# Optimization experiments

Hardware: AMD Instinct MI355X
Metric: run time of the kernel (lower is better)

The kernel has to match this reference:

```python
import jax, jax.numpy as jnp
import numpy as np

N, H, F, E, K = 2048, 1024, 4096, 8, 2


def setup_inputs() -> dict:
    key = jax.random.key(0)
    ks = jax.random.split(key, 6)
    x = jax.random.normal(ks[0], (N, H), dtype=jnp.float32)
    mapping = jax.random.randint(ks[1], (N, K), 0, E)
    Wg = jax.random.normal(ks[2], (E, H), dtype=jnp.float32) * (1.0 / np.sqrt(H))
    W1 = jax.random.normal(ks[3], (E, H, F), dtype=jnp.float32) * (1.0 / np.sqrt(H))
    b1 = jnp.zeros((E, F), dtype=jnp.float32)
    W2 = jax.random.normal(ks[4], (E, F, H), dtype=jnp.float32) * (1.0 / np.sqrt(F))
    b2 = jnp.zeros((E, H), dtype=jnp.float32)
    return {"x": x, "mapping": mapping, "Wg": Wg, "W1": W1, "b1": b1, "W2": W2, "b2": b2}


def reference(x, mapping, Wg, W1, b1, W2, b2):
    # Gate logits: note original applies softmax over dim=0 (the token axis).
    logits = jax.nn.softmax(x @ Wg.T, axis=0)  # [N, E]

    # Per-expert MLP. Original sorts tokens by expert, runs per-expert GEMMs on
    # dynamic splits, then unsorts -- mathematically: y[i,k] = MLP_{mapping[i,k]}(x[i]).
    # JIT-friendly dense baseline: run every expert over all tokens, gather per token.
    def mlp(e):
        h = jax.nn.gelu(x @ W1[e] + b1[e])  # [N, F]
        return h @ W2[e] + b2[e]            # [N, H]

    y_all = jnp.stack([mlp(e) for e in range(E)])  # [E, N, H]

    # Gate weights gathered per (token, k), normalized over top-k.
    w = jnp.take_along_axis(logits, mapping, axis=1)  # [N, K]
    w = w / jnp.sum(w, axis=-1, keepdims=True)

    idx = jnp.arange(x.shape[0])
    out = jnp.zeros_like(x)
    for k in range(mapping.shape[1]):
        yk = y_all[mapping[:, k], idx]  # [N, H] gather per token's k-th expert
        out = out + yk * w[:, k:k + 1]
    return out
```

## Files before the change

kernel.cpp:

```cpp
#include <hip/hip_runtime.h>

#define N_TOK 2048
#define HD    1024
#define FD    4096
#define NE    8

typedef __attribute__((ext_vector_type(8))) short short8;
typedef __attribute__((ext_vector_type(4))) float floatx4;

__device__ __forceinline__ unsigned short f2bf(float f) {
  unsigned int u = __float_as_uint(f);
  u += 0x7fffu + ((u >> 16) & 1u);
  return (unsigned short)(u >> 16);
}

__device__ __forceinline__ void gl2lds16(const unsigned short* g, unsigned short* l) {
  __builtin_amdgcn_global_load_lds(
      (const __attribute__((address_space(1))) unsigned int*)g,
      (__attribute__((address_space(3))) unsigned int*)l, 16, 0, 0);
}

__device__ __forceinline__ float gelu_tanh(float x) {
  float t = 0.7978845608028654f * x * (1.0f + 0.044715f * x * x);
  return 0.5f * x * (1.0f + tanhf(t));
}

__device__ __forceinline__ int poff_of(const int* __restrict__ cnt, int e) {
  int o = 0;
  for (int i = 0; i < e; ++i) o += (cnt[i] + 127) & ~127;
  return o;
}

__global__ void k_gating(const float* __restrict__ x, const float* __restrict__ wg,
                         float* __restrict__ p) {
  int wave = threadIdx.x >> 6;
  int lane = threadIdx.x & 63;
  int n = blockIdx.x * 4 + wave;
  const float4* xr = (const float4*)(x + (size_t)n * HD);
  float4 xv[4];
  #pragma unroll
  for (int i = 0; i < 4; ++i) xv[i] = xr[lane + i * 64];
  for (int e = 0; e < NE; ++e) {
    const float4* wr = (const float4*)(wg + (size_t)e * HD);
    float s = 0.f;
    #pragma unroll
    for (int i = 0; i < 4; ++i) {
      float4 w4 = wr[lane + i * 64];
      s += xv[i].x * w4.x + xv[i].y * w4.y + xv[i].z * w4.z + xv[i].w * w4.w;
    }
    for (int o = 32; o > 0; o >>= 1) s += __shfl_xor(s, o, 64);
    if (lane == 0) p[e * N_TOK + n] = s;
  }
}

__global__ void k_softmax(float* __restrict__ p) {
  int e = blockIdx.x;
  float* col = p + e * N_TOK;
  __shared__ float red[256];
  int t = threadIdx.x;
  float m = -1e30f;
  for (int i = t; i < N_TOK; i += 256) m = fmaxf(m, col[i]);
  red[t] = m; __syncthreads();
  for (int s = 128; s > 0; s >>= 1) { if (t < s) red[t] = fmaxf(red[t], red[t + s]); __syncthreads(); }
  m = red[0]; __syncthreads();
  float sum = 0.f;
  for (int i = t; i < N_TOK; i += 256) { float v = expf(col[i] - m); col[i] = v; sum += v; }
  red[t] = sum; __syncthreads();
  for (int s = 128; s > 0; s >>= 1) { if (t < s) red[t] += red[t + s]; __syncthreads(); }
  float inv = 1.0f / red[0];
  for (int i = t; i < N_TOK; i += 256) col[i] *= inv;
}

__global__ void k_route(const int* __restrict__ mp, const float* __restrict__ p,
                        int* __restrict__ cnt, int* __restrict__ idxl,
                        int* __restrict__ tke, int* __restrict__ tks, float* __restrict__ tkw) {
  int n = blockIdx.x * 256 + threadIdx.x;
  if (n >= N_TOK) return;
  int m0 = mp[n * 2 + 0], m1 = mp[n * 2 + 1];
  if (m0 == m1) {
    int s = atomicAdd(&cnt[m0], 1);
    idxl[m0 * N_TOK + s] = n;
    tke[n * 2] = m0; tks[n * 2] = s; tkw[n * 2] = 1.0f;
    tke[n * 2 + 1] = m0; tks[n * 2 + 1] = s; tkw[n * 2 + 1] = 0.0f;
  } else {
    float p0 = p[m0 * N_TOK + n], p1 = p[m1 * N_TOK + n];
    float inv = 1.0f / (p0 + p1);
    int s0 = atomicAdd(&cnt[m0], 1);
    idxl[m0 * N_TOK + s0] = n;
    tke[n * 2] = m0; tks[n * 2] = s0; tkw[n * 2] = p0 * inv;
    int s1 = atomicAdd(&cnt[m1], 1);
    idxl[m1 * N_TOK + s1] = n;
    tke[n * 2 + 1] = m1; tks[n * 2 + 1] = s1; tkw[n * 2 + 1] = p1 * inv;
  }
}

__global__ void k_gather(const float* __restrict__ x, const int* __restrict__ cnt,
                         const int* __restrict__ idxl, unsigned short* __restrict__ xg) {
  int e = blockIdx.y;
  int r = blockIdx.x;
  int c = cnt[e];
  int pc = (c + 127) & ~127;
  if (r >= pc) return;
  unsigned short* dst = xg + ((size_t)poff_of(cnt, e) + r) * HD;
  int t = threadIdx.x;
  union { unsigned short us[8]; uint4 v; } o;
  if (r < c) {
    const float* src = x + (size_t)idxl[e * N_TOK + r] * HD;
    float4 f0 = ((const float4*)src)[t * 2];
    float4 f1 = ((const float4*)src)[t * 2 + 1];
    o.us[0] = f2bf(f0.x); o.us[1] = f2bf(f0.y); o.us[2] = f2bf(f0.z); o.us[3] = f2bf(f0.w);
    o.us[4] = f2bf(f1.x); o.us[5] = f2bf(f1.y); o.us[6] = f2bf(f1.z); o.us[7] = f2bf(f1.w);
  } else {
    o.v.x = 0u; o.v.y = 0u; o.v.z = 0u; o.v.w = 0u;
  }
  ((uint4*)dst)[t] = o.v;
}

__global__ __launch_bounds__(256) void k_transcvt2(const float* __restrict__ w1,
                                                   unsigned short* __restrict__ w1t,
                                                   const float* __restrict__ w2,
                                                   unsigned short* __restrict__ w2t) {
  __shared__ float tile[64][65];
  int l = blockIdx.x;
  const float* src; unsigned short* dst; int rows, cols, bx, by, e;
  if (l < 8192) {
    src = w1; dst = w1t; rows = HD; cols = FD;
    bx = l & 63; by = (l >> 6) & 15; e = l >> 10;
  } else {
    int l2 = l - 8192;
    src = w2; dst = w2t; rows = FD; cols = HD;
    bx = l2 & 15; by = (l2 >> 4) & 63; e = l2 >> 10;
  }
  const size_t base = (size_t)e * rows * cols;
  int c0 = bx * 64, r0 = by * 64;
  int t = threadIdx.x;
  int lr = t >> 4;
  int lc = (t & 15) * 4;
  #pragma unroll
  for (int i = 0; i < 64; i += 16) {
    float4 v = *(const float4*)(src + base + (size_t)(r0 + lr + i) * cols + c0 + lc);
    tile[lr + i][lc] = v.x; tile[lr + i][lc + 1] = v.y;
    tile[lr + i][lc + 2] = v.z; tile[lr + i][lc + 3] = v.w;
  }
  __syncthreads();
  int oc = t >> 2;
  int rseg = (t & 3) * 16;
  union { unsigned short us[16]; uint4 v[2]; } o;
  #pragma unroll
  for (int i = 0; i < 16; ++i) o.us[i] = f2bf(tile[rseg + i][oc]);
  unsigned short* d = dst + base + (size_t)(c0 + oc) * rows + r0 + rseg;
  ((uint4*)d)[0] = o.v[0];
  ((uint4*)d)[1] = o.v[1];
}

__global__ __launch_bounds__(256) void k_gemm1(
    const unsigned short* __restrict__ xg, const unsigned short* __restrict__ w1t,
    const float* __restrict__ b1, const int* __restrict__ cnt,
    unsigned short* __restrict__ h) {
  const int l = blockIdx.x;
  const int mt = l >> 5;
  const int nt = l & 31;
  const int mbase = mt * 128;
  const int nbase = nt * 128;

  int e = -1;
  {
    int o = 0;
    #pragma unroll
    for (int i = 0; i < NE; ++i) {
      int ci = cnt[i];
      int pc = (ci + 127) & ~127;
      if (mbase >= o && mbase < o + pc) e = i;
      o += pc;
    }
  }
  if (e < 0) return;

  const unsigned short* A = xg + (size_t)mbase * HD;
  const unsigned short* B = w1t + ((size_t)e * FD + nbase) * HD;

  __shared__ unsigned short As[128 * 32];
  __shared__ unsigned short Bs[128 * 32];

  const int tid = threadIdx.x;
  const int wave = tid >> 6, lane = tid & 63;
  const int quad = lane >> 4, lrow = lane & 15;
  const int wm = (wave >> 1) * 64, wn = (wave & 1) * 64;

  floatx4 acc[4][4];
  #pragma unroll
  for (int i = 0; i < 4; ++i)
    #pragma unroll
    for (int j = 0; j < 4; ++j) acc[i][j] = (floatx4){0.f, 0.f, 0.f, 0.f};

  const int r0 = tid >> 2, k0 = (tid & 3) * 8;

  for (int kt = 0; kt < HD / 32; ++kt) {
    __syncthreads();
    const unsigned short* ga = A + kt * 32;
    const unsigned short* gb = B + kt * 32;
    gl2lds16(ga + (size_t)r0 * HD + k0,        As + (size_t)(wave * 64) * 8);
    gl2lds16(ga + (size_t)(64 + r0) * HD + k0, As + (size_t)(256 + wave * 64) * 8);
    gl2lds16(gb + (size_t)r0 * HD + k0,        Bs + (size_t)(wave * 64) * 8);
    gl2lds16(gb + (size_t)(64 + r0) * HD + k0, Bs + (size_t)(256 + wave * 64) * 8);
    __syncthreads();
    short8 aF[4], bF[4];
    #pragma unroll
    for (int i = 0; i < 4; ++i)
      aF[i] = *(const short8*)(As + (wm + i * 16 + lrow) * 32 + quad * 8);
    #pragma unroll
    for (int j = 0; j < 4; ++j)
      bF[j] = *(const short8*)(Bs + (wn + j * 16 + lrow) * 32 + quad * 8);
    #pragma unroll
    for (int i = 0; i < 4; ++i)
      #pragma unroll
      for (int j = 0; j < 4; ++j)
        acc[i][j] = __builtin_amdgcn_mfma_f32_16x16x32_bf16(aF[i], bF[j], acc[i][j], 0, 0, 0);
  }

  #pragma unroll
  for (int i = 0; i < 4; ++i) {
    #pragma unroll
    for (int rr = 0; rr < 4; ++rr) {
      int row = mbase + wm + i * 16 + quad * 4 + rr;
      unsigned short* hr = h + (size_t)row * FD + nbase;
      #pragma unroll
      for (int j = 0; j < 4; ++j) {
        int col = wn + j * 16 + lrow;
        float v = acc[i][j][rr] + b1[e * FD + nbase + col];
        hr[col] = f2bf(gelu_tanh(v));
      }
    }
  }
}

__global__ __launch_bounds__(256) void k_gemm2(
    const unsigned short* __restrict__ h, const unsigned short* __restrict__ w2t,
    const int* __restrict__ cnt, unsigned short* __restrict__ ya) {
  const int l = blockIdx.x;
  const int mt = l >> 3;
  const int nt = l & 7;
  const int mbase = mt * 128;
  const int nbase = nt * 128;

  int e = -1;
  {
    int o = 0;
    #pragma unroll
    for (int i = 0; i < NE; ++i) {
      int ci = cnt[i];
      int pc = (ci + 127) & ~127;
      if (mbase >= o && mbase < o + pc) e = i;
      o += pc;
    }
  }
  if (e < 0) return;

  const unsigned short* A = h + (size_t)mbase * FD;
  const unsigned short* B = w2t + ((size_t)e * HD + nbase) * FD;

  __shared__ unsigned short As[128 * 32];
  __shared__ unsigned short Bs[128 * 32];

  const int tid = threadIdx.x;
  const int wave = tid >> 6, lane = tid & 63;
  const int quad = lane >> 4, lrow = lane & 15;
  const int wm = (wave >> 1) * 64, wn = (wave & 1) * 64;

  floatx4 acc[4][4];
  #pragma unroll
  for (int i = 0; i < 4; ++i)
    #pragma unroll
    for (int j = 0; j < 4; ++j) acc[i][j] = (floatx4){0.f, 0.f, 0.f, 0.f};

  const int r0 = tid >> 2, k0 = (tid & 3) * 8;

  for (int kt = 0; kt < FD / 32; ++kt) {
    __syncthreads();
    const unsigned short* ga = A + kt * 32;
    const unsigned short* gb = B + kt * 32;
    gl2lds16(ga + (size_t)r0 * FD + k0,        As + (size_t)(wave * 64) * 8);
    gl2lds16(ga + (size_t)(64 + r0) * FD + k0, As + (size_t)(256 + wave * 64) * 8);
    gl2lds16(gb + (size_t)r0 * FD + k0,        Bs + (size_t)(wave * 64) * 8);
    gl2lds16(gb + (size_t)(64 + r0) * FD + k0, Bs + (size_t)(256 + wave * 64) * 8);
    __syncthreads();
    short8 aF[4], bF[4];
    #pragma unroll
    for (int i = 0; i < 4; ++i)
      aF[i] = *(const short8*)(As + (wm + i * 16 + lrow) * 32 + quad * 8);
    #pragma unroll
    for (int j = 0; j < 4; ++j)
      bF[j] = *(const short8*)(Bs + (wn + j * 16 + lrow) * 32 + quad * 8);
    #pragma unroll
    for (int i = 0; i < 4; ++i)
      #pragma unroll
      for (int j = 0; j < 4; ++j)
        acc[i][j] = __builtin_amdgcn_mfma_f32_16x16x32_bf16(aF[i], bF[j], acc[i][j], 0, 0, 0);
  }

  #pragma unroll
  for (int i = 0; i < 4; ++i) {
    #pragma unroll
    for (int rr = 0; rr < 4; ++rr) {
      int row = mbase + wm + i * 16 + quad * 4 + rr;
      unsigned short* yr = ya + (size_t)row * HD + nbase;
      #pragma unroll
      for (int j = 0; j < 4; ++j) {
        int col = wn + j * 16 + lrow;
        yr[col] = f2bf(acc[i][j][rr]);
      }
    }
  }
}

__global__ __launch_bounds__(256) void k_combine(
    const unsigned short* __restrict__ ya, const float* __restrict__ b2,
    const int* __restrict__ cnt, const int* __restrict__ tke,
    const int* __restrict__ tks, const float* __restrict__ tkw,
    float* __restrict__ out) {
  int n = blockIdx.x;
  int e0 = tke[n * 2], e1 = tke[n * 2 + 1];
  int p0 = poff_of(cnt, e0) + tks[n * 2];
  int p1 = poff_of(cnt, e1) + tks[n * 2 + 1];
  float w0 = tkw[n * 2], w1 = tkw[n * 2 + 1];
  int c = threadIdx.x * 4;
  union { unsigned short us[4]; ushort2 u2[2]; unsigned long long ll; } y0, y1;
  y0.ll = *(const unsigned long long*)(ya + (size_t)p0 * HD + c);
  y1.ll = *(const unsigned long long*)(ya + (size_t)p1 * HD + c);
  float4 bb0 = *(const float4*)(b2 + (size_t)e0 * HD + c);
  float4 bb1 = *(const float4*)(b2 + (size_t)e1 * HD + c);
  float4 o;
  o.x = w0 * (__uint_as_float((unsigned)y0.us[0] << 16) + bb0.x) + w1 * (__uint_as_float((unsigned)y1.us[0] << 16) + bb1.x);
  o.y = w0 * (__uint_as_float((unsigned)y0.us[1] << 16) + bb0.y) + w1 * (__uint_as_float((unsigned)y1.us[1] << 16) + bb1.y);
  o.z = w0 * (__uint_as_float((unsigned)y0.us[2] << 16) + bb0.z) + w1 * (__uint_as_float((unsigned)y1.us[2] << 16) + bb1.z);
  o.w = w0 * (__uint_as_float((unsigned)y0.us[3] << 16) + bb0.w) + w1 * (__uint_as_float((unsigned)y1.us[3] << 16) + bb1.w);
  *(float4*)(out + (size_t)n * HD + c) = o;
}

extern "C" void kernel_launch(void* const* d_in, const int* in_sizes, int n_in,
                              void* d_out, int out_size, void* d_ws, size_t ws_size,
                              hipStream_t stream) {
  const float* x  = (const float*)d_in[0];
  const int*   mp = (const int*)d_in[1];
  const float* wg = (const float*)d_in[2];
  const float* w1 = (const float*)d_in[3];
  const float* b1 = (const float*)d_in[4];
  const float* w2 = (const float*)d_in[5];
  const float* b2 = (const float*)d_in[6];
  float* out = (float*)d_out;
  char* ws = (char*)d_ws;

  float* p    = (float*)(ws + 0);
  int*   cnt  = (int*)(ws + 65536);
  int*   idxl = (int*)(ws + 66048);
  int*   tke  = (int*)(ws + 131584);
  int*   tks  = (int*)(ws + 147968);
  float* tkw  = (float*)(ws + 164352);
  size_t off = 180736;
  unsigned short* w1t = (unsigned short*)(ws + off);  off += 67108864;
  unsigned short* w2t = (unsigned short*)(ws + off);  off += 67108864;
  unsigned short* xg  = (unsigned short*)(ws + off);  off += 10485760;
  unsigned short* h   = (unsigned short*)(ws + off);  off += 41943040;
  unsigned short* ya  = (unsigned short*)(ws + off);  off += 10485760;

  hipMemsetAsync(cnt, 0, 32, stream);

  k_gating<<<512, 256, 0, stream>>>(x, wg, p);
  k_softmax<<<NE, 256, 0, stream>>>(p);
  k_route<<<NE, 256, 0, stream>>>(mp, p, cnt, idxl, tke, tks, tkw);
  k_transcvt2<<<16384, 256, 0, stream>>>(w1, w1t, w2, w2t);
  k_gather<<<dim3(N_TOK, NE), 128, 0, stream>>>(x, cnt, idxl, xg);
  k_gemm1<<<1280, 256, 0, stream>>>(xg, w1t, b1, cnt, h);
  k_gemm2<<<320, 256, 0, stream>>>(h, w2t, cnt, ya);
  k_combine<<<N_TOK, 256, 0, stream>>>(ya, b2, cnt, tke, tks, tkw, out);
}
```

Measured before the change: 526.7 us.

## Pre-tile transposed bf16 weights into MFMA-ready blocks and retile gemm2

```diff
diff --git a/kernel.cpp b/kernel.cpp
--- a/kernel.cpp
+++ b/kernel.cpp
@@ -116,41 +116,48 @@
   ((uint4*)dst)[t] = o.v;
 }
 
-__global__ __launch_bounds__(256) void k_transcvt2(const float* __restrict__ w1,
+__global__ __launch_bounds__(256) void k_transtile(const float* __restrict__ w1,
                                                    unsigned short* __restrict__ w1t,
                                                    const float* __restrict__ w2,
                                                    unsigned short* __restrict__ w2t) {
-  __shared__ float tile[64][65];
+  __shared__ unsigned short lt[32 * 264];
   int l = blockIdx.x;
-  const float* src; unsigned short* dst; int rows, cols, bx, by, e;
-  if (l < 8192) {
-    src = w1; dst = w1t; rows = HD; cols = FD;
-    bx = l & 63; by = (l >> 6) & 15; e = l >> 10;
+  const float* src; unsigned short* dst; int ncols; size_t tb0, tb1;
+  int kt, ng;
+  if (l < 4096) {
+    int e = l >> 9; kt = (l >> 4) & 31; ng = l & 15;
+    src = w1 + (size_t)e * HD * FD; ncols = FD; dst = w1t;
+    tb0 = (((size_t)e * 32 + ng * 2 + 0) * 32 + kt) * 4096;
+    tb1 = (((size_t)e * 32 + ng * 2 + 1) * 32 + kt) * 4096;
   } else {
-    int l2 = l - 8192;
-    src = w2; dst = w2t; rows = FD; cols = HD;
-    bx = l2 & 15; by = (l2 >> 4) & 63; e = l2 >> 10;
-  }
-  const size_t base = (size_t)e * rows * cols;
-  int c0 = bx * 64, r0 = by * 64;
-  int t = threadIdx.x;
-  int lr = t >> 4;
-  int lc = (t & 15) * 4;
-  #pragma unroll
-  for (int i = 0; i < 64; i += 16) {
-    float4 v = *(const float4*)(src + base + (size_t)(r0 + lr + i) * cols + c0 + lc);
-    tile[lr + i][lc] = v.x; tile[lr + i][lc + 1] = v.y;
-    tile[lr + i][lc + 2] = v.z; tile[lr + i][lc + 3] = v.w;
+    int l2 = l - 4096;
+    int e = l2 >> 9; kt = (l2 >> 2) & 127; ng = l2 & 3;
+    src = w2 + (size_t)e * FD * HD; ncols = HD; dst = w2t;
+    tb0 = (((size_t)e * 8 + ng * 2 + 0) * 128 + kt) * 4096;
+    tb1 = (((size_t)e * 8 + ng * 2 + 1) * 128 + kt) * 4096;
+  }
+  const int t = threadIdx.x;
+  #pragma unroll
+  for (int p = 0; p < 8; ++p) {
+    int f = p * 256 + t;
+    int r = f >> 6;
+    int c4 = f & 63;
+    float4 v = *(const float4*)(src + (size_t)(kt * 32 + r) * ncols + ng * 256 + c4 * 4);
+    union { unsigned short us[4]; unsigned long long ll; } u;
+    u.us[0] = f2bf(v.x); u.us[1] = f2bf(v.y); u.us[2] = f2bf(v.z); u.us[3] = f2bf(v.w);
+    *(unsigned long long*)(lt + r * 264 + c4 * 4) = u.ll;
   }
   __syncthreads();
-  int oc = t >> 2;
-  int rseg = (t & 3) * 16;
-  union { unsigned short us[16]; uint4 v[2]; } o;
-  #pragma unroll
-  for (int i = 0; i < 16; ++i) o.us[i] = f2bf(tile[rseg + i][oc]);
-  unsigned short* d = dst + base + (size_t)(c0 + oc) * rows + r0 + rseg;
-  ((uint4*)d)[0] = o.v[0];
-  ((uint4*)d)[1] = o.v[1];
+  #pragma unroll
+  for (int q = 0; q < 4; ++q) {
+    int c = q * 256 + t;
+    int n = c >> 2, kc = c & 3;
+    union { unsigned short us[8]; uint4 v; } u;
+    #pragma unroll
+    for (int j = 0; j < 8; ++j) u.us[j] = lt[(kc * 8 + j) * 264 + n];
+    size_t tb = (q < 2) ? tb0 : tb1;
+    *(uint4*)(dst + tb + (size_t)(n & 127) * 32 + kc * 8) = u.v;
+  }
 }
 
 __global__ __launch_bounds__(256) void k_gemm1(
@@ -163,21 +170,22 @@
   const int mbase = mt * 128;
   const int nbase = nt * 128;
 
-  int e = -1;
+  int e = -1, po = 0, ce = 0;
   {
     int o = 0;
     #pragma unroll
     for (int i = 0; i < NE; ++i) {
       int ci = cnt[i];
       int pc = (ci + 127) & ~127;
-      if (mbase >= o && mbase < o + pc) e = i;
+      if (mbase >= o && mbase < o + pc) { e = i; po = o; ce = ci; }
       o += pc;
     }
   }
   if (e < 0) return;
+  if (mbase - po >= ce) return;
 
   const unsigned short* A = xg + (size_t)mbase * HD;
-  const unsigned short* B = w1t + ((size_t)e * FD + nbase) * HD;
+  const unsigned short* Bt = w1t + (((size_t)e * 32 + nt) * 32) * 4096;
 
   __shared__ unsigned short As[128 * 32];
   __shared__ unsigned short Bs[128 * 32];
@@ -193,16 +201,16 @@
     #pragma unroll
     for (int j = 0; j < 4; ++j) acc[i][j] = (floatx4){0.f, 0.f, 0.f, 0.f};
 
-  const int r0 = tid >> 2, k0 = (tid & 3) * 8;
+  const int rA = tid >> 2, kA = (tid & 3) * 8;
 
   for (int kt = 0; kt < HD / 32; ++kt) {
     __syncthreads();
     const unsigned short* ga = A + kt * 32;
-    const unsigned short* gb = B + kt * 32;
-    gl2lds16(ga + (size_t)r0 * HD + k0,        As + (size_t)(wave * 64) * 8);
-    gl2lds16(ga + (size_t)(64 + r0) * HD + k0, As + (size_t)(256 + wave * 64) * 8);
-    gl2lds16(gb + (size_t)r0 * HD + k0,        Bs + (size_t)(wave * 64) * 8);
-    gl2lds16(gb + (size_t)(64 + r0) * HD + k0, Bs + (size_t)(256 + wave * 64) * 8);
+    gl2lds16(ga + (size_t)rA * HD + kA,        As + (size_t)wave * 512);
+    gl2lds16(ga + (size_t)(64 + rA) * HD + kA, As + 2048 + (size_t)wave * 512);
+    const unsigned short* gb = Bt + (size_t)kt * 4096 + (size_t)tid * 8;
+    gl2lds16(gb,        Bs + (size_t)wave * 512);
+    gl2lds16(gb + 2048, Bs + 2048 + (size_t)wave * 512);
     __syncthreads();
     short8 aF[4], bF[4];
     #pragma unroll
@@ -238,64 +246,71 @@
     const unsigned short* __restrict__ h, const unsigned short* __restrict__ w2t,
     const int* __restrict__ cnt, unsigned short* __restrict__ ya) {
   const int l = blockIdx.x;
-  const int mt = l >> 3;
-  const int nt = l & 7;
+  const int mt = l >> 4;
+  const int nt = l & 15;
   const int mbase = mt * 128;
-  const int nbase = nt * 128;
-
-  int e = -1;
+  const int nbase = nt * 64;
+
+  int e = -1, po = 0, ce = 0;
   {
     int o = 0;
     #pragma unroll
     for (int i = 0; i < NE; ++i) {
       int ci = cnt[i];
       int pc = (ci + 127) & ~127;
-      if (mbase >= o && mbase < o + pc) e = i;
+      if (mbase >= o && mbase < o + pc) { e = i; po = o; ce = ci; }
       o += pc;
     }
   }
   if (e < 0) return;
+  if (mbase - po >= ce) return;
 
   const unsigned short* A = h + (size_t)mbase * FD;
-  const unsigned short* B = w2t + ((size_t)e * HD + nbase) * FD;
-
-  __shared__ unsigned short As[128 * 32];
-  __shared__ unsigned short Bs[128 * 32];
+  const unsigned short* Bt = w2t + (((size_t)e * 8 + (nt >> 1)) * 128) * 4096
+                                 + (size_t)(nt & 1) * 2048;
+
+  __shared__ unsigned short As[2][128 * 32];
+  __shared__ unsigned short Bs[2][64 * 32];
 
   const int tid = threadIdx.x;
   const int wave = tid >> 6, lane = tid & 63;
   const int quad = lane >> 4, lrow = lane & 15;
-  const int wm = (wave >> 1) * 64, wn = (wave & 1) * 64;
-
-  floatx4 acc[4][4];
+  const int wm = (wave >> 1) * 64, wn = (wave & 1) * 32;
+
+  floatx4 acc[4][2];
   #pragma unroll
   for (int i = 0; i < 4; ++i)
     #pragma unroll
-    for (int j = 0; j < 4; ++j) acc[i][j] = (floatx4){0.f, 0.f, 0.f, 0.f};
-
-  const int r0 = tid >> 2, k0 = (tid & 3) * 8;
-
-  for (int kt = 0; kt < FD / 32; ++kt) {
+    for (int j = 0; j < 2; ++j) acc[i][j] = (floatx4){0.f, 0.f, 0.f, 0.f};
+
+  const int rA = tid >> 2, kA = (tid & 3) * 8;
+
+  for (int kt = 0; kt < FD / 64; ++kt) {
     __syncthreads();
-    const unsigned short* ga = A + kt * 32;
-    const unsigned short* gb = B + kt * 32;
-    gl2lds16(ga + (size_t)r0 * FD + k0,        As + (size_t)(wave * 64) * 8);
-    gl2lds16(ga + (size_t)(64 + r0) * FD + k0, As + (size_t)(256 + wave * 64) * 8);
-    gl2lds16(gb + (size_t)r0 * FD + k0,        Bs + (size_t)(wave * 64) * 8);
-    gl2lds16(gb + (size_t)(64 + r0) * FD + k0, Bs + (size_t)(256 + wave * 64) * 8);
+    #pragma unroll
+    for (int cc = 0; cc < 2; ++cc) {
+      int kk = kt * 2 + cc;
+      const unsigned short* ga = A + kk * 32;
+      gl2lds16(ga + (size_t)rA * FD + kA,        As[cc] + (size_t)wave * 512);
+      gl2lds16(ga + (size_t)(64 + rA) * FD + kA, As[cc] + 2048 + (size_t)wave * 512);
+      gl2lds16(Bt + (size_t)kk * 4096 + (size_t)tid * 8, Bs[cc] + (size_t)wave * 512);
+    }
     __syncthreads();
-    short8 aF[4], bF[4];
-    #pragma unroll
-    for (int i = 0; i < 4; ++i)
-      aF[i] = *(const short8*)(As + (wm + i * 16 + lrow) * 32 + quad * 8);
-    #pragma unroll
-    for (int j = 0; j < 4; ++j)
-      bF[j] = *(const short8*)(Bs + (wn + j * 16 + lrow) * 32 + quad * 8);
-    #pragma unroll
-    for (int i = 0; i < 4; ++i)
-      #pragma unroll
-      for (int j = 0; j < 4; ++j)
-        acc[i][j] = __builtin_amdgcn_mfma_f32_16x16x32_bf16(aF[i], bF[j], acc[i][j], 0, 0, 0);
+    #pragma unroll
+    for (int cc = 0; cc < 2; ++cc) {
+      short8 aF[4], bF[2];
+      #pragma unroll
+      for (int i = 0; i < 4; ++i)
+        aF[i] = *(const short8*)(As[cc] + (wm + i * 16 + lrow) * 32 + quad * 8);
+      #pragma unroll
+      for (int j = 0; j < 2; ++j)
+        bF[j] = *(const short8*)(Bs[cc] + (wn + j * 16 + lrow) * 32 + quad * 8);
+      #pragma unroll
+      for (int i = 0; i < 4; ++i)
+        #pragma unroll
+        for (int j = 0; j < 2; ++j)
+          acc[i][j] = __builtin_amdgcn_mfma_f32_16x16x32_bf16(aF[i], bF[j], acc[i][j], 0, 0, 0);
+    }
   }
 
   #pragma unroll
@@ -305,7 +320,7 @@
       int row = mbase + wm + i * 16 + quad * 4 + rr;
       unsigned short* yr = ya + (size_t)row * HD + nbase;
       #pragma unroll
-      for (int j = 0; j < 4; ++j) {
+      for (int j = 0; j < 2; ++j) {
         int col = wn + j * 16 + lrow;
         yr[col] = f2bf(acc[i][j][rr]);
       }
@@ -324,7 +339,7 @@
   int p1 = poff_of(cnt, e1) + tks[n * 2 + 1];
   float w0 = tkw[n * 2], w1 = tkw[n * 2 + 1];
   int c = threadIdx.x * 4;
-  union { unsigned short us[4]; ushort2 u2[2]; unsigned long long ll; } y0, y1;
+  union { unsigned short us[4]; unsigned long long ll; } y0, y1;
   y0.ll = *(const unsigned long long*)(ya + (size_t)p0 * HD + c);
   y1.ll = *(const unsigned long long*)(ya + (size_t)p1 * HD + c);
   float4 bb0 = *(const float4*)(b2 + (size_t)e0 * HD + c);
@@ -368,9 +383,9 @@
   k_gating<<<512, 256, 0, stream>>>(x, wg, p);
   k_softmax<<<NE, 256, 0, stream>>>(p);
   k_route<<<NE, 256, 0, stream>>>(mp, p, cnt, idxl, tke, tks, tkw);
-  k_transcvt2<<<16384, 256, 0, stream>>>(w1, w1t, w2, w2t);
+  k_transtile<<<8192, 256, 0, stream>>>(w1, w1t, w2, w2t);
   k_gather<<<dim3(N_TOK, NE), 128, 0, stream>>>(x, cnt, idxl, xg);
   k_gemm1<<<1280, 256, 0, stream>>>(xg, w1t, b1, cnt, h);
-  k_gemm2<<<320, 256, 0, stream>>>(h, w2t, cnt, ya);
+  k_gemm2<<<640, 256, 0, stream>>>(h, w2t, cnt, ya);
   k_combine<<<N_TOK, 256, 0, stream>>>(ya, b2, cnt, tke, tks, tkw, out);
 }
```

Result: faster. 506.2 us (-3.9%).
